# Optimization experiments

Hardware: AMD Instinct MI355X
Metric: run time of the kernel (lower is better)

The kernel has to match this reference:

```python
import jax, jax.numpy as jnp
import numpy as np

N_NODES = 100000
N_EDGES = 3200000


def setup_inputs() -> dict:
    key = jax.random.key(0)
    ks = jax.random.split(key, 12)
    x = jax.random.normal(ks[0], (N_NODES, 34), dtype=jnp.float32)
    edge_index = jax.random.randint(ks[1], (2, N_EDGES), 0, N_NODES, dtype=jnp.int64)
    def lin(k, fin, fout):
        s = 1.0 / np.sqrt(fin)
        kw, kb = jax.random.split(k)
        W = jax.random.uniform(kw, (fin, fout), jnp.float32, -s, s)
        b = jax.random.uniform(kb, (fout,), jnp.float32, -s, s)
        return W, b
    W1, b1 = lin(ks[2], 34, 64)
    W2, b2 = lin(ks[3], 64, 32)
    W3, b3 = lin(ks[4], 32, 16)
    W4, b4 = lin(ks[5], 16, 8)
    Wc, bc = lin(ks[6], 8, 2)
    return {"x": x, "edge_index": edge_index,
            "W1": W1, "b1": b1, "W2": W2, "b2": b2,
            "W3": W3, "b3": b3, "W4": W4, "b4": b4,
            "Wc": Wc, "bc": bc}


def _gcn_norm(edge_index, n_nodes):
    # PyG GCNConv: add self-loops, symmetric normalization D^-1/2 (A+I) D^-1/2
    loop = jnp.arange(n_nodes, dtype=edge_index.dtype)
    src = jnp.concatenate([edge_index[0], loop])  # [E+N]
    dst = jnp.concatenate([edge_index[1], loop])
    deg = jax.ops.segment_sum(jnp.ones_like(dst, dtype=jnp.float32), dst,
                              num_segments=n_nodes)
    dinv = jnp.where(deg > 0, jax.lax.rsqrt(deg), 0.0)
    norm = dinv[src] * dinv[dst]  # [E+N]
    return src, dst, norm


def _gcn_conv(h, W, b, src, dst, norm, n_nodes):
    h = h @ W                                    # [N, Fout] small GEMM
    msg = h[src] * norm[:, None]                 # gather + scale
    out = jax.ops.segment_sum(msg, dst, num_segments=n_nodes)  # scatter-add
    return out + b


def reference(x, edge_index, W1, b1, W2, b2, W3, b3, W4, b4, Wc, bc):
    n = x.shape[0]
    src, dst, norm = _gcn_norm(edge_index, n)
    h = jnp.tanh(_gcn_conv(x, W1, b1, src, dst, norm, n))
    h = jnp.tanh(_gcn_conv(h, W2, b2, src, dst, norm, n))
    h = jnp.tanh(_gcn_conv(h, W3, b3, src, dst, norm, n))
    h = jnp.tanh(_gcn_conv(h, W4, b4, src, dst, norm, n))
    out = h @ Wc + bc
    return (out, h)
```

## Files before the change

### kernel.cpp

```cpp
#include <hip/hip_runtime.h>
#include <math.h>

#define N_NODES 100000
#define BSHIFT 8
#define BNODES 256
#define NB ((N_NODES + BNODES - 1) / BNODES)
#define CHUNK 8192


__device__ __forceinline__ unsigned short f2bf(float x) {
    unsigned u = __float_as_uint(x);
    u += 0x7FFFu + ((u >> 16) & 1u);
    return (unsigned short)(u >> 16);
}
__device__ __forceinline__ unsigned pack2(float a, float b) {
    return (unsigned)f2bf(a) | ((unsigned)f2bf(b) << 16);
}
__device__ __forceinline__ float bflo(unsigned u) { return __uint_as_float(u << 16); }
__device__ __forceinline__ float bfhi(unsigned u) { return __uint_as_float(u & 0xFFFF0000u); }
__device__ __forceinline__ int nt_ld(const int* p) { return __builtin_nontemporal_load(p); }


__global__ __launch_bounds__(256) void bucket_count(const int* __restrict__ dst,
                                                    int* __restrict__ bucketCount, int E) {
    __shared__ int hist[NB];
    for (int i = threadIdx.x; i < NB; i += 256) hist[i] = 0;
    __syncthreads();
    int i = blockIdx.x * blockDim.x + threadIdx.x;
    int stride = gridDim.x * blockDim.x;
    for (int e = i; e < E; e += stride)
        atomicAdd(&hist[nt_ld(dst + e) >> BSHIFT], 1);
    __syncthreads();
    for (int i2 = threadIdx.x; i2 < NB; i2 += 256) {
        int c = hist[i2];
        if (c) atomicAdd(&bucketCount[i2], c);
    }
}


__global__ __launch_bounds__(512) void bucket_scan(const int* __restrict__ bucketCount,
                                                   int* __restrict__ bucketOff,
                                                   int* __restrict__ bucketCursor, int E) {
    __shared__ int sh[512];
    int t = threadIdx.x;
    int v = (t < NB) ? bucketCount[t] : 0;
    sh[t] = v;
    __syncthreads();
    for (int d = 1; d < 512; d <<= 1) {
        int u = (t >= d) ? sh[t - d] : 0;
        __syncthreads();
        sh[t] += u;
        __syncthreads();
    }
    if (t < NB) { bucketOff[t] = sh[t] - v; bucketCursor[t] = sh[t] - v; }
    if (t == 0) bucketOff[NB] = E;
}


__global__ __launch_bounds__(256) void bucket_fill(const int* __restrict__ src,
                                                   const int* __restrict__ dst,
                                                   int* __restrict__ bucketCursor,
                                                   unsigned int* __restrict__ binned, int E) {
    __shared__ int hist[NB];
    __shared__ int base[NB];
    __shared__ int lcur[NB];
    __shared__ unsigned int recs[CHUNK];
    __shared__ unsigned short bkt[CHUNK];
    int t = threadIdx.x;
    for (int i = t; i < NB; i += 256) { hist[i] = 0; lcur[i] = 0; }
    __syncthreads();
    int cbase = blockIdx.x * CHUNK;
#pragma unroll
    for (int j = 0; j < CHUNK / 256; ++j) {
        int slot = t + j * 256;
        int e = cbase + slot;
        if (e < E) {
            int s = nt_ld(src + e);
            int d = nt_ld(dst + e);
            recs[slot] = (unsigned)s | ((unsigned)(d & (BNODES - 1)) << 17);
            int b = d >> BSHIFT;
            bkt[slot] = (unsigned short)b;
            atomicAdd(&hist[b], 1);
        } else {
            bkt[slot] = 0xFFFF;
        }
    }
    __syncthreads();
    for (int i = t; i < NB; i += 256) {
        int c = hist[i];
        base[i] = c ? atomicAdd(&bucketCursor[i], c) : 0;
    }
    __syncthreads();
#pragma unroll
    for (int j = 0; j < CHUNK / 256; ++j) {
        int slot = t + j * 256;
        unsigned short b = bkt[slot];
        if (b != 0xFFFF) {
            int pos = base[b] + atomicAdd(&lcur[b], 1);
            binned[pos] = recs[slot];
        }
    }
}


__global__ __launch_bounds__(256) void node_off_sort(const unsigned int* __restrict__ binned,
                                                     const int* __restrict__ bucketOff,
                                                     int* __restrict__ off,
                                                     float* __restrict__ dinv,
                                                     int* __restrict__ srcs, int n, int E) {
    __shared__ int hist[BNODES];
    __shared__ int sh[BNODES];
    __shared__ int lcur[BNODES];
    int t = threadIdx.x;
    int b = blockIdx.x;
    hist[t] = 0;
    __syncthreads();
    int rb = bucketOff[b], re = bucketOff[b + 1];
    for (int e = rb + t; e < re; e += 256)
        atomicAdd(&hist[(binned[e] >> 17) & 255], 1);
    __syncthreads();
    int v = hist[t];
    sh[t] = v;
    __syncthreads();
    for (int d = 1; d < 256; d <<= 1) {
        int u = (t >= d) ? sh[t - d] : 0;
        __syncthreads();
        sh[t] += u;
        __syncthreads();
    }
    int base = rb + sh[t] - v;
    lcur[t] = base;
    int g = b * BNODES + t;
    if (g < n) {
        off[g] = base;
        dinv[g] = rsqrtf((float)v + 1.0f);
    }
    if (b == NB - 1 && t == 0) off[n] = E;
    __syncthreads();
    for (int e = rb + t; e < re; e += 256) {
        unsigned int r = binned[e];
        int pos = atomicAdd(&lcur[(r >> 17) & 255], 1);
        srcs[pos] = (int)(r & 0x1FFFF);
    }
}


__global__ void x_pack(const float* __restrict__ x, const float* __restrict__ dinv,
                       unsigned* __restrict__ xm, unsigned* __restrict__ xt, int n) {
    int i = blockIdx.x * blockDim.x + threadIdx.x;
    if (i >= n) return;
    float dv = dinv[i];
    const float2* xr = (const float2*)(x + (size_t)i * 34);
    unsigned* om = xm + (size_t)i * 16;
#pragma unroll
    for (int j = 0; j < 16; ++j) { float2 v = xr[j]; om[j] = pack2(dv * v.x, dv * v.y); }
    float2 v = xr[16];
    xt[i] = pack2(dv * v.x, dv * v.y);
}


__global__ __launch_bounds__(256) void gather_x_bf16(const int* __restrict__ off,
        const int* __restrict__ srcs, const unsigned* __restrict__ xm,
        const unsigned* __restrict__ xt, const float* __restrict__ dinv,
        float* __restrict__ aggx, int n) {
    int g = blockIdx.x * 16 + (threadIdx.x >> 4);
    int f = threadIdx.x & 15;
    if (g >= n) return;
    int rb = off[g], re = off[g + 1];
    unsigned ug = xm[(size_t)g * 16 + f];
    float a0 = bflo(ug), a1 = bfhi(ug);
    float a2 = 0.f, a3 = 0.f;
    if (f == 0) { unsigned tt = xt[g]; a2 = bflo(tt); a3 = bfhi(tt); }
    int e = rb;
    for (; e + 8 <= re; e += 8) {
        int s0 = nt_ld(srcs + e),     s1 = nt_ld(srcs + e + 1);
        int s2 = nt_ld(srcs + e + 2), s3 = nt_ld(srcs + e + 3);
        int s4 = nt_ld(srcs + e + 4), s5 = nt_ld(srcs + e + 5);
        int s6 = nt_ld(srcs + e + 6), s7 = nt_ld(srcs + e + 7);
        unsigned u0 = xm[(size_t)s0 * 16 + f], u1 = xm[(size_t)s1 * 16 + f];
        unsigned u2 = xm[(size_t)s2 * 16 + f], u3 = xm[(size_t)s3 * 16 + f];
        unsigned u4 = xm[(size_t)s4 * 16 + f], u5 = xm[(size_t)s5 * 16 + f];
        unsigned u6 = xm[(size_t)s6 * 16 + f], u7 = xm[(size_t)s7 * 16 + f];
        a0 += bflo(u0); a1 += bfhi(u0); a0 += bflo(u1); a1 += bfhi(u1);
        a0 += bflo(u2); a1 += bfhi(u2); a0 += bflo(u3); a1 += bfhi(u3);
        a0 += bflo(u4); a1 += bfhi(u4); a0 += bflo(u5); a1 += bfhi(u5);
        a0 += bflo(u6); a1 += bfhi(u6); a0 += bflo(u7); a1 += bfhi(u7);
        if (f == 0) {
            unsigned t0 = xt[s0], t1 = xt[s1], t2 = xt[s2], t3 = xt[s3];
            unsigned t4 = xt[s4], t5 = xt[s5], t6 = xt[s6], t7 = xt[s7];
            a2 += bflo(t0); a3 += bfhi(t0); a2 += bflo(t1); a3 += bfhi(t1);
            a2 += bflo(t2); a3 += bfhi(t2); a2 += bflo(t3); a3 += bfhi(t3);
            a2 += bflo(t4); a3 += bfhi(t4); a2 += bflo(t5); a3 += bfhi(t5);
            a2 += bflo(t6); a3 += bfhi(t6); a2 += bflo(t7); a3 += bfhi(t7);
        }
    }
    for (; e < re; ++e) {
        int s = nt_ld(srcs + e);
        unsigned u = xm[(size_t)s * 16 + f];
        a0 += bflo(u); a1 += bfhi(u);
        if (f == 0) { unsigned tt = xt[s]; a2 += bflo(tt); a3 += bfhi(tt); }
    }
    float dv = dinv[g];
    *(float2*)(aggx + (size_t)g * 34 + 2 * f) = make_float2(dv * a0, dv * a1);
    if (f == 0) *(float2*)(aggx + (size_t)g * 34 + 32) = make_float2(dv * a2, dv * a3);
}


#define G12_BLOCKS 1024

__global__ __launch_bounds__(256) void gemm12(const float* __restrict__ aggx,
        const float* __restrict__ W1, const float* __restrict__ b1,
        const float* __restrict__ W2, const float* __restrict__ dinv,
        unsigned* __restrict__ linh2, int n) {
    __shared__ float sW1[34 * 64];
    __shared__ float sW2[64 * 32];
    __shared__ float sh1[4][64];
    for (int i = threadIdx.x; i < 34 * 64; i += 256) sW1[i] = W1[i];
    for (int i = threadIdx.x; i < 64 * 32; i += 256) sW2[i] = W2[i];
    __syncthreads();
    int r = threadIdx.x / 64;
    int j = threadIdx.x % 64;
    float bj = b1[j];
    for (int base = blockIdx.x * 4; base < n; base += G12_BLOCKS * 4) {
        int row = base + r;
        float h1v = 0.f;
        if (row < n) {
            const float* hr = aggx + (size_t)row * 34;
            float acc = 0.f;
#pragma unroll
            for (int k = 0; k < 34; ++k) acc = fmaf(hr[k], sW1[k * 64 + j], acc);
            h1v = tanhf(acc + bj);
        }
        sh1[r][j] = h1v;
        __syncthreads();
        if (row < n && j < 16) {
            float a0 = 0.f, a1 = 0.f;
#pragma unroll
            for (int k = 0; k < 64; ++k) {
                float v = sh1[r][k];
                a0 = fmaf(v, sW2[k * 32 + 2 * j], a0);
                a1 = fmaf(v, sW2[k * 32 + 2 * j + 1], a1);
            }
            float dv = dinv[row];
            linh2[(size_t)row * 16 + j] = pack2(dv * a0, dv * a1);
        }
        __syncthreads();
    }
}


__global__ __launch_bounds__(256) void gather2_proj(const int* __restrict__ off,
        const int* __restrict__ srcs, const unsigned* __restrict__ linh2,
        const float* __restrict__ dinv, const float* __restrict__ b2,
        const float* __restrict__ W3, unsigned* __restrict__ linh3, int n) {
    __shared__ float sW3[32 * 16];
    for (int i = threadIdx.x; i < 32 * 16; i += 256) sW3[i] = W3[i];
    __syncthreads();
    int g = blockIdx.x * 16 + (threadIdx.x >> 4);
    int f = threadIdx.x & 15;
    if (g >= n) return;
    int rb = off[g], re = off[g + 1];
    unsigned ug = linh2[(size_t)g * 16 + f];
    float a0 = bflo(ug), a1 = bfhi(ug);
    int e = rb;
    for (; e + 8 <= re; e += 8) {
        int s0 = nt_ld(srcs + e),     s1 = nt_ld(srcs + e + 1);
        int s2 = nt_ld(srcs + e + 2), s3 = nt_ld(srcs + e + 3);
        int s4 = nt_ld(srcs + e + 4), s5 = nt_ld(srcs + e + 5);
        int s6 = nt_ld(srcs + e + 6), s7 = nt_ld(srcs + e + 7);
        unsigned u0 = linh2[(size_t)s0 * 16 + f], u1 = linh2[(size_t)s1 * 16 + f];
        unsigned u2 = linh2[(size_t)s2 * 16 + f], u3 = linh2[(size_t)s3 * 16 + f];
        unsigned u4 = linh2[(size_t)s4 * 16 + f], u5 = linh2[(size_t)s5 * 16 + f];
        unsigned u6 = linh2[(size_t)s6 * 16 + f], u7 = linh2[(size_t)s7 * 16 + f];
        a0 += bflo(u0); a1 += bfhi(u0); a0 += bflo(u1); a1 += bfhi(u1);
        a0 += bflo(u2); a1 += bfhi(u2); a0 += bflo(u3); a1 += bfhi(u3);
        a0 += bflo(u4); a1 += bfhi(u4); a0 += bflo(u5); a1 += bfhi(u5);
        a0 += bflo(u6); a1 += bfhi(u6); a0 += bflo(u7); a1 += bfhi(u7);
    }
    for (; e < re; ++e) {
        int s = nt_ld(srcs + e);
        unsigned u = linh2[(size_t)s * 16 + f];
        a0 += bflo(u); a1 += bfhi(u);
    }
    float dv = dinv[g];
    float h0 = tanhf(fmaf(dv, a0, b2[2 * f]));
    float h1 = tanhf(fmaf(dv, a1, b2[2 * f + 1]));
    float p[16];
#pragma unroll
    for (int o = 0; o < 16; ++o)
        p[o] = h0 * sW3[(2 * f) * 16 + o] + h1 * sW3[(2 * f + 1) * 16 + o];
#pragma unroll
    for (int m = 1; m <= 8; m <<= 1)
#pragma unroll
        for (int o = 0; o < 16; ++o) p[o] += __shfl_xor(p[o], m);
    if (f < 8) linh3[(size_t)g * 8 + f] = pack2(dv * p[2 * f], dv * p[2 * f + 1]);
}


__global__ __launch_bounds__(256) void gather3_proj(const int* __restrict__ off,
        const int* __restrict__ srcs, const unsigned* __restrict__ linh3,
        const float* __restrict__ dinv, const float* __restrict__ b3,
        const float* __restrict__ W4, unsigned* __restrict__ linh4, int n) {
    __shared__ float sW4[16 * 8];
    for (int i = threadIdx.x; i < 16 * 8; i += 256) sW4[i] = W4[i];
    __syncthreads();
    int g = blockIdx.x * 32 + (threadIdx.x >> 3);
    int f = threadIdx.x & 7;
    if (g >= n) return;
    int rb = off[g], re = off[g + 1];
    unsigned ug = linh3[(size_t)g * 8 + f];
    float a0 = bflo(ug), a1 = bfhi(ug);
    int e = rb;
    for (; e + 8 <= re; e += 8) {
        int s0 = nt_ld(srcs + e),     s1 = nt_ld(srcs + e + 1);
        int s2 = nt_ld(srcs + e + 2), s3 = nt_ld(srcs + e + 3);
        int s4 = nt_ld(srcs + e + 4), s5 = nt_ld(srcs + e + 5);
        int s6 = nt_ld(srcs + e + 6), s7 = nt_ld(srcs + e + 7);
        unsigned u0 = linh3[(size_t)s0 * 8 + f], u1 = linh3[(size_t)s1 * 8 + f];
        unsigned u2 = linh3[(size_t)s2 * 8 + f], u3 = linh3[(size_t)s3 * 8 + f];
        unsigned u4 = linh3[(size_t)s4 * 8 + f], u5 = linh3[(size_t)s5 * 8 + f];
        unsigned u6 = linh3[(size_t)s6 * 8 + f], u7 = linh3[(size_t)s7 * 8 + f];
        a0 += bflo(u0); a1 += bfhi(u0); a0 += bflo(u1); a1 += bfhi(u1);
        a0 += bflo(u2); a1 += bfhi(u2); a0 += bflo(u3); a1 += bfhi(u3);
        a0 += bflo(u4); a1 += bfhi(u4); a0 += bflo(u5); a1 += bfhi(u5);
        a0 += bflo(u6); a1 += bfhi(u6); a0 += bflo(u7); a1 += bfhi(u7);
    }
    for (; e < re; ++e) {
        int s = nt_ld(srcs + e);
        unsigned u = linh3[(size_t)s * 8 + f];
        a0 += bflo(u); a1 += bfhi(u);
    }
    float dv = dinv[g];
    float h0 = tanhf(fmaf(dv, a0, b3[2 * f]));
    float h1 = tanhf(fmaf(dv, a1, b3[2 * f + 1]));
    float p[8];
#pragma unroll
    for (int o = 0; o < 8; ++o)
        p[o] = h0 * sW4[(2 * f) * 8 + o] + h1 * sW4[(2 * f + 1) * 8 + o];
#pragma unroll
    for (int m = 1; m <= 4; m <<= 1)
#pragma unroll
        for (int o = 0; o < 8; ++o) p[o] += __shfl_xor(p[o], m);
    if (f < 4) linh4[(size_t)g * 4 + f] = pack2(dv * p[2 * f], dv * p[2 * f + 1]);
}


__global__ __launch_bounds__(256) void gather4_cls(const int* __restrict__ off,
        const int* __restrict__ srcs, const unsigned* __restrict__ linh4,
        const float* __restrict__ dinv, const float* __restrict__ b4,
        float* __restrict__ hout, const float* __restrict__ Wc,
        const float* __restrict__ bc, float* __restrict__ out, int n) {
    int g = blockIdx.x * 64 + (threadIdx.x >> 2);
    int f = threadIdx.x & 3;
    if (g >= n) return;
    int rb = off[g], re = off[g + 1];
    unsigned ug = linh4[(size_t)g * 4 + f];
    float a0 = bflo(ug), a1 = bfhi(ug);
    int e = rb;
    for (; e + 8 <= re; e += 8) {
        int s0 = nt_ld(srcs + e),     s1 = nt_ld(srcs + e + 1);
        int s2 = nt_ld(srcs + e + 2), s3 = nt_ld(srcs + e + 3);
        int s4 = nt_ld(srcs + e + 4), s5 = nt_ld(srcs + e + 5);
        int s6 = nt_ld(srcs + e + 6), s7 = nt_ld(srcs + e + 7);
        unsigned u0 = linh4[(size_t)s0 * 4 + f], u1 = linh4[(size_t)s1 * 4 + f];
        unsigned u2 = linh4[(size_t)s2 * 4 + f], u3 = linh4[(size_t)s3 * 4 + f];
        unsigned u4 = linh4[(size_t)s4 * 4 + f], u5 = linh4[(size_t)s5 * 4 + f];
        unsigned u6 = linh4[(size_t)s6 * 4 + f], u7 = linh4[(size_t)s7 * 4 + f];
        a0 += bflo(u0); a1 += bfhi(u0); a0 += bflo(u1); a1 += bfhi(u1);
        a0 += bflo(u2); a1 += bfhi(u2); a0 += bflo(u3); a1 += bfhi(u3);
        a0 += bflo(u4); a1 += bfhi(u4); a0 += bflo(u5); a1 += bfhi(u5);
        a0 += bflo(u6); a1 += bfhi(u6); a0 += bflo(u7); a1 += bfhi(u7);
    }
    for (; e < re; ++e) {
        int s = nt_ld(srcs + e);
        unsigned u = linh4[(size_t)s * 4 + f];
        a0 += bflo(u); a1 += bfhi(u);
    }
    float dv = dinv[g];
    a0 = tanhf(fmaf(dv, a0, b4[2 * f]));
    a1 = tanhf(fmaf(dv, a1, b4[2 * f + 1]));
    *(float2*)(hout + (size_t)g * 8 + 2 * f) = make_float2(a0, a1);
    float p0 = a0 * Wc[4 * f]     + a1 * Wc[4 * f + 2];
    float p1 = a0 * Wc[4 * f + 1] + a1 * Wc[4 * f + 3];
    p0 += __shfl_xor(p0, 1); p1 += __shfl_xor(p1, 1);
    p0 += __shfl_xor(p0, 2); p1 += __shfl_xor(p1, 2);
    if (f == 0) {
        out[(size_t)g * 2]     = p0 + bc[0];
        out[(size_t)g * 2 + 1] = p1 + bc[1];
    }
}


static inline char* alignp(char* p) {
    return (char*)(((uintptr_t)p + 15) & ~(uintptr_t)15);
}

extern "C" void kernel_launch(void* const* d_in, const int* in_sizes, int n_in,
                              void* d_out, int out_size, void* d_ws, size_t ws_size,
                              hipStream_t stream) {
    const float* x  = (const float*)d_in[0];
    const int*   ei = (const int*)d_in[1];
    const float* W1 = (const float*)d_in[2];  const float* b1 = (const float*)d_in[3];
    const float* W2 = (const float*)d_in[4];
    const float* b2 = (const float*)d_in[5];
    const float* W3 = (const float*)d_in[6];  const float* b3 = (const float*)d_in[7];
    const float* W4 = (const float*)d_in[8];  const float* b4 = (const float*)d_in[9];
    const float* Wc = (const float*)d_in[10]; const float* bc = (const float*)d_in[11];

    float* out  = (float*)d_out;
    float* hout = out + (size_t)2 * N_NODES;

    const int n = N_NODES;
    const int E = in_sizes[1] / 2;
    const int* src = ei;
    const int* dst = ei + E;

    char* w = (char*)d_ws;
    float*        dinv         = (float*)w;        w = alignp(w + (size_t)n * 4);
    int*          bucketCount  = (int*)w;          w = alignp(w + (size_t)NB * 4);
    int*          bucketOff    = (int*)w;          w = alignp(w + (size_t)(NB + 1) * 4);
    int*          bucketCursor = (int*)w;          w = alignp(w + (size_t)NB * 4);
    int*          off          = (int*)w;          w = alignp(w + (size_t)(n + 1) * 4);
    unsigned int* binned       = (unsigned int*)w; w = alignp(w + (size_t)E * 4);
    int*          srcs         = (int*)w;          w = alignp(w + (size_t)E * 4);
    unsigned int* xm           = (unsigned int*)w; w = alignp(w + (size_t)n * 16 * 4);
    unsigned int* xt           = (unsigned int*)w; w = alignp(w + (size_t)n * 4);
    float*        aggx         = (float*)w;        w = alignp(w + (size_t)n * 34 * 4);
    unsigned int* linh2        = (unsigned int*)w; w = alignp(w + (size_t)n * 16 * 4);
    unsigned int* linh3        = (unsigned int*)w; w = alignp(w + (size_t)n * 8 * 4);
    unsigned int* linh4        = (unsigned int*)w; w = alignp(w + (size_t)n * 4 * 4);

    hipMemsetAsync(bucketCount, 0, NB * sizeof(int), stream);
    bucket_count<<<1024, 256, 0, stream>>>(dst, bucketCount, E);
    bucket_scan<<<1, 512, 0, stream>>>(bucketCount, bucketOff, bucketCursor, E);
    bucket_fill<<<(E + CHUNK - 1) / CHUNK, 256, 0, stream>>>(src, dst, bucketCursor, binned, E);
    node_off_sort<<<NB, 256, 0, stream>>>(binned, bucketOff, off, dinv, srcs, n, E);
    x_pack<<<(n + 255) / 256, 256, 0, stream>>>(x, dinv, xm, xt, n);

    gather_x_bf16<<<(n + 15) / 16, 256, 0, stream>>>(off, srcs, xm, xt, dinv, aggx, n);
    gemm12<<<G12_BLOCKS, 256, 0, stream>>>(aggx, W1, b1, W2, dinv, linh2, n);

    gather2_proj<<<(n + 15) / 16, 256, 0, stream>>>(off, srcs, linh2, dinv, b2, W3, linh3, n);

    gather3_proj<<<(n + 31) / 32, 256, 0, stream>>>(off, srcs, linh3, dinv, b3, W4, linh4, n);

    gather4_cls<<<(n + 63) / 64, 256, 0, stream>>>(off, srcs, linh4, dinv, b4, hout,
                                                   Wc, bc, out, n);
}
```

Before: 510.6 us.

## Restructure gemm12 to process 16 rows per iteration with all threads busy

The fused layer-1/layer-2 dense kernel now handles 16 rows per block iteration instead of 4. Each thread computes four first-layer outputs, and all 256 threads take part in the second-layer projection, where previously only 16 of every 64 did. W1 is stored transposed in shared memory so weights and activations can be read as float2, and the grid is doubled. This cuts idle lanes and barrier count per row, at the cost of more shared memory and possible bank conflicts on the transposed, stride-34 W1 reads.

```diff
diff --git a/kernel.cpp b/kernel.cpp
--- a/kernel.cpp
+++ b/kernel.cpp
@@ -206,43 +206,65 @@
 }
 
 
-#define G12_BLOCKS 1024
+#define G12_BLOCKS 2048
 
 __global__ __launch_bounds__(256) void gemm12(const float* __restrict__ aggx,
         const float* __restrict__ W1, const float* __restrict__ b1,
         const float* __restrict__ W2, const float* __restrict__ dinv,
         unsigned* __restrict__ linh2, int n) {
-    __shared__ float sW1[34 * 64];
+    __shared__ float sW1t[64 * 34];
     __shared__ float sW2[64 * 32];
-    __shared__ float sh1[4][64];
-    for (int i = threadIdx.x; i < 34 * 64; i += 256) sW1[i] = W1[i];
+    __shared__ float sh1[16][64];
+    for (int i = threadIdx.x; i < 34 * 64; i += 256) {
+        int k = i >> 6, j = i & 63;
+        sW1t[j * 34 + k] = W1[i];
+    }
     for (int i = threadIdx.x; i < 64 * 32; i += 256) sW2[i] = W2[i];
     __syncthreads();
-    int r = threadIdx.x / 64;
-    int j = threadIdx.x % 64;
+    int j  = threadIdx.x & 63;
+    int rq = threadIdx.x >> 6;
+    int p  = threadIdx.x & 15;
+    int r2 = threadIdx.x >> 4;
     float bj = b1[j];
-    for (int base = blockIdx.x * 4; base < n; base += G12_BLOCKS * 4) {
-        int row = base + r;
-        float h1v = 0.f;
-        if (row < n) {
-            const float* hr = aggx + (size_t)row * 34;
-            float acc = 0.f;
-#pragma unroll
-            for (int k = 0; k < 34; ++k) acc = fmaf(hr[k], sW1[k * 64 + j], acc);
-            h1v = tanhf(acc + bj);
+    const float2* w1v = (const float2*)(sW1t + j * 34);
+    const float2* w2v = (const float2*)sW2;
+    for (int base = blockIdx.x * 16; base < n; base += G12_BLOCKS * 16) {
+#pragma unroll
+        for (int q = 0; q < 4; ++q) {
+            int r = rq * 4 + q;
+            int row = base + r;
+            float h1v = 0.f;
+            if (row < n) {
+                const float2* hr = (const float2*)(aggx + (size_t)row * 34);
+                float acc = 0.f;
+#pragma unroll
+                for (int k2 = 0; k2 < 17; ++k2) {
+                    float2 wv = w1v[k2];
+                    float2 hv = hr[k2];
+                    acc = fmaf(hv.x, wv.x, acc);
+                    acc = fmaf(hv.y, wv.y, acc);
+                }
+                h1v = tanhf(acc + bj);
+            }
+            sh1[r][j] = h1v;
         }
-        sh1[r][j] = h1v;
-        __syncthreads();
-        if (row < n && j < 16) {
-            float a0 = 0.f, a1 = 0.f;
-#pragma unroll
-            for (int k = 0; k < 64; ++k) {
-                float v = sh1[r][k];
-                a0 = fmaf(v, sW2[k * 32 + 2 * j], a0);
-                a1 = fmaf(v, sW2[k * 32 + 2 * j + 1], a1);
+        __syncthreads();
+        {
+            int row = base + r2;
+            if (row < n) {
+                const float2* sh1v = (const float2*)&sh1[r2][0];
+                float a0 = 0.f, a1 = 0.f;
+#pragma unroll
+                for (int k2 = 0; k2 < 32; ++k2) {
+                    float2 h = sh1v[k2];
+                    float2 wa = w2v[(2 * k2) * 16 + p];
+                    float2 wb = w2v[(2 * k2 + 1) * 16 + p];
+                    a0 = fmaf(h.x, wa.x, a0); a1 = fmaf(h.x, wa.y, a1);
+                    a0 = fmaf(h.y, wb.x, a0); a1 = fmaf(h.y, wb.y, a1);
+                }
+                float dv = dinv[row];
+                linh2[(size_t)row * 16 + p] = pack2(dv * a0, dv * a1);
             }
-            float dv = dinv[row];
-            linh2[(size_t)row * 16 + j] = pack2(dv * a0, dv * a1);
         }
         __syncthreads();
     }
```

Measured after the change: 470.2 us. 7.9% less time.
